# Performance work log

Hardware: AMD Instinct MI355X
Metric: run time of the kernel (lower is better)

Reference implementation:

```python
import jax, jax.numpy as jnp
import numpy as np

NX, NY, NZ = 432, 496, 1
VX, VY, VZ = 0.16, 0.16, 4.0
XOFF = VX / 2 + 0.0
YOFF = VY / 2 + (-39.68)
ZOFF = VZ / 2 + (-3.0)
GRID = NZ * NX * NY
P, NPT, B = 100000, 32, 8
EPS = 1e-3


def setup_inputs() -> dict:
    key = jax.random.key(0)
    k1, k2, k3, k4 = jax.random.split(key, 4)
    voxels = jax.random.normal(k1, (P, NPT, 4), dtype=jnp.float32)
    num_points = jax.random.randint(k2, (P,), 1, NPT + 1, dtype=jnp.int32)
    b = jax.random.randint(k3, (P,), 0, B, dtype=jnp.int32)
    # unique BEV cells (17 coprime with GRID, P < GRID) -> deterministic scatter
    cell = (jnp.arange(P, dtype=jnp.int32) * 17) % GRID
    y = cell // NX
    x = cell % NX
    coords = jnp.stack([b, jnp.zeros_like(b), y, x], axis=1)  # [P,4] (b,z,y,x)
    W = jax.random.normal(k4, (64, 10), dtype=jnp.float32) * 0.1
    gamma = jnp.ones((64,), dtype=jnp.float32)
    beta = jnp.zeros((64,), dtype=jnp.float32)
    return {"voxels": voxels, "num_points": num_points, "coords": coords,
            "W": W, "gamma": gamma, "beta": beta}


def reference(voxels, num_points, coords, W, gamma, beta):
    cf = coords.astype(voxels.dtype)
    npf = num_points.astype(voxels.dtype)
    # cluster feature: offset from pillar mean
    points_mean = voxels[:, :, :3].sum(axis=1, keepdims=True) / npf[:, None, None]
    f_cluster = voxels[:, :, :3] - points_mean
    # center feature: offset from voxel center
    cx = cf[:, 3, None] * VX + XOFF
    cy = cf[:, 2, None] * VY + YOFF
    cz = cf[:, 1, None] * VZ + ZOFF
    f_center = jnp.stack([voxels[:, :, 0] - cx,
                          voxels[:, :, 1] - cy,
                          voxels[:, :, 2] - cz], axis=-1)
    feat = jnp.concatenate([voxels, f_cluster, f_center], axis=-1)  # [P,N,10]
    mask = (jnp.arange(NPT, dtype=jnp.int32)[None, :] < num_points[:, None])
    feat = feat * mask.astype(feat.dtype)[:, :, None]
    # linear(10->64, no bias) + BatchNorm1d (batch stats, biased var) + relu
    x = jnp.einsum('pnf,cf->pnc', feat, W)  # [P,N,64]
    mean = x.mean(axis=(0, 1))
    var = ((x - mean) ** 2).mean(axis=(0, 1))
    x = (x - mean) * jax.lax.rsqrt(var + EPS) * gamma + beta
    x = jax.nn.relu(x)
    pillars = x.max(axis=1)  # [P,64]
    idx = coords[:, 1] + coords[:, 2] * NX + coords[:, 3]
    bev = jnp.zeros((B, GRID, 64), dtype=pillars.dtype)
    bev = bev.at[coords[:, 0], idx].set(pillars)
    bev = jnp.transpose(bev, (0, 2, 1))  # [B,64,GRID]
    return bev.reshape(B, 64 * NZ, NY, NX)
```

## Files before the change

kernel.cpp:

```cpp
#include <hip/hip_runtime.h>

typedef unsigned short u16;
typedef unsigned uint2n __attribute__((ext_vector_type(2)));
typedef float float4n __attribute__((ext_vector_type(4)));

#define NXg 432
#define NYg 496
#define GRIDg (NXg*NYg)
#define NPTg 32
#define Bg 8
#define CHg 64
#define NSLOT 32

__device__ __forceinline__ float bf2f(u16 u){
    union { unsigned int i; float f; } x; x.i = ((unsigned int)u) << 16; return x.f;
}
__device__ __forceinline__ u16 f2bf(float f){
    union { float f; unsigned int i; } x; x.f = f;
    unsigned int i = x.i + 0x7FFFu + ((x.i >> 16) & 1u);
    return (u16)(i >> 16);
}
__device__ __forceinline__ bool is_bf16(const void* gamma){
    return ((*(const unsigned*)gamma) & 0xFFFFu) != 0u;
}

__global__ __launch_bounds__(256) void pfe_init(int* __restrict__ map, float* __restrict__ chsum){
    int t = blockIdx.x*256 + threadIdx.x;
    ((int4*)map)[t] = make_int4(-1,-1,-1,-1);
    if (t < (NSLOT*128)/4) ((float4*)chsum)[t] = make_float4(0.f,0.f,0.f,0.f);
}

__global__ __launch_bounds__(256) void pfe_pillar(
    const void* __restrict__ vox, const int* __restrict__ nump,
    const int* __restrict__ coords, const void* __restrict__ Wv,
    const void* __restrict__ gv,
    void* __restrict__ pv, int* __restrict__ map, float* __restrict__ chsum,
    int P, int nwaves)
{
    const bool isbf = is_bf16(gv);
    int lane = threadIdx.x & 63;
    int wl   = __builtin_amdgcn_readfirstlane(threadIdx.x >> 6);
    int wid  = blockIdx.x*4 + wl;
    int n    = lane & 31;

    float w4,w5,w6,w7,w8,w9, wp0,wp1,wp2,wp3;
    bool gsel;
    {
        float w[10];
#pragma unroll
        for (int j=0;j<10;j++)
            w[j] = isbf ? bf2f(((const u16*)Wv)[lane*10 + j]) : ((const float*)Wv)[lane*10 + j];
        wp0 = w[0]+w[4]+w[7];
        wp1 = w[1]+w[5]+w[8];
        wp2 = w[2]+w[6]+w[9];
        wp3 = w[3];
        w4=w[4]; w5=w[5]; w6=w[6]; w7=w[7]; w8=w[8]; w9=w[9];
        float g = isbf ? bf2f(((const u16*)gv)[lane]) : ((const float*)gv)[lane];
        gsel = (g >= 0.f);
    }

    float sx = 0.f, sx2 = 0.f;

    for (int p = wid; p < P; p += nwaves) {
        int np = nump[p];
        int4 cc = *(const int4*)(coords + 4*p);

        float4 pt;
        if (isbf){
            ushort4 raw = *(const ushort4*)((const u16*)vox + ((size_t)p*NPTg + n)*4);
            pt = make_float4(bf2f(raw.x), bf2f(raw.y), bf2f(raw.z), bf2f(raw.w));
        } else {
            pt = *(const float4*)((const float*)vox + ((size_t)p*NPTg + n)*4);
        }
        float s0 = pt.x, s1 = pt.y, s2 = pt.z;
#pragma unroll
        for (int m = 1; m < 32; m <<= 1){
            s0 += __shfl_xor(s0, m, 64);
            s1 += __shfl_xor(s1, m, 64);
            s2 += __shfl_xor(s2, m, 64);
        }
        float inv = 1.0f / (float)np;
        float m0 = s0*inv, m1 = s1*inv, m2 = s2*inv;
        float ccx = (float)cc.w * 0.16f + 0.08f;
        float ccy = (float)cc.z * 0.16f + (0.08f - 39.68f);
        float ccz = (float)cc.y * 4.0f  + (2.0f - 3.0f);
        float d = -(m0*w4 + m1*w5 + m2*w6 + ccx*w7 + ccy*w8 + ccz*w9);

        float qmx = -3e38f, qmn = 3e38f, sq = 0.f, sq2 = 0.f;
#define PROC(ax,ay,az,aw) { \
        float q = fmaf((ax), wp0, fmaf((ay), wp1, fmaf((az), wp2, (aw)*wp3))); \
        qmx = fmaxf(qmx, q); qmn = fminf(qmn, q); \
        sq += q; sq2 = fmaf(q, q, sq2); }
        if (isbf){
            const ushort4* rg = (const ushort4*)vox + (size_t)p*NPTg;
            int k = 0;
            for (; k + 4 <= np; k += 4){
                ushort4 r0 = rg[k+0], r1 = rg[k+1], r2 = rg[k+2], r3 = rg[k+3];
                PROC(bf2f(r0.x), bf2f(r0.y), bf2f(r0.z), bf2f(r0.w));
                PROC(bf2f(r1.x), bf2f(r1.y), bf2f(r1.z), bf2f(r1.w));
                PROC(bf2f(r2.x), bf2f(r2.y), bf2f(r2.z), bf2f(r2.w));
                PROC(bf2f(r3.x), bf2f(r3.y), bf2f(r3.z), bf2f(r3.w));
            }
            for (; k < np; k++){
                ushort4 r = rg[k];
                PROC(bf2f(r.x), bf2f(r.y), bf2f(r.z), bf2f(r.w));
            }
        } else {
            const float4* rg = (const float4*)vox + (size_t)p*NPTg;
            int k = 0;
            for (; k + 4 <= np; k += 4){
                float4 a0 = rg[k+0], a1 = rg[k+1], a2 = rg[k+2], a3 = rg[k+3];
                PROC(a0.x,a0.y,a0.z,a0.w);
                PROC(a1.x,a1.y,a1.z,a1.w);
                PROC(a2.x,a2.y,a2.z,a2.w);
                PROC(a3.x,a3.y,a3.z,a3.w);
            }
            for (; k < np; k++){
                float4 a = rg[k];
                PROC(a.x,a.y,a.z,a.w);
            }
        }
#undef PROC

        float npf = (float)np;
        sx  += sq + npf*d;
        sx2 += sq2 + d*(2.f*sq + npf*d);

        float fmx = qmx + d, fmn = qmn + d;
        if (np < NPTg){ fmx = fmaxf(fmx, 0.f); fmn = fminf(fmn, 0.f); }
        float sel = gsel ? fmx : fmn;
        if (isbf) ((u16*)pv)[(size_t)p*CHg + lane] = f2bf(sel);
        else      ((float*)pv)[(size_t)p*CHg + lane] = sel;
        if (lane == 0) map[cc.x*GRIDg + cc.z*NXg + cc.w] = p;
    }

    float* slot = chsum + (blockIdx.x & (NSLOT-1))*128;
    atomicAdd(slot + lane, sx);
    atomicAdd(slot + 64 + lane, sx2);
}

__global__ __launch_bounds__(64) void pfe_stats(
    const float* __restrict__ chsum,
    const void* __restrict__ gv, const void* __restrict__ bv,
    float* __restrict__ sb, int P)
{
    const bool isbf = is_bf16(gv);
    int t = threadIdx.x;
    float S = 0.f, S2 = 0.f;
    for (int sl = 0; sl < NSLOT; sl++){
        S  += chsum[sl*128 + t];
        S2 += chsum[sl*128 + 64 + t];
    }
    float cnt = (float)P * (float)NPTg;
    float mean = S / cnt;
    float var  = S2 / cnt - mean*mean;
    float g  = isbf ? bf2f(((const u16*)gv)[t]) : ((const float*)gv)[t];
    float be = isbf ? bf2f(((const u16*)bv)[t]) : ((const float*)bv)[t];
    float sc = g * rsqrtf(var + 1e-3f);
    sb[t] = sc; sb[64 + t] = be - mean*sc;
}

__global__ __launch_bounds__(192) void pfe_gather(
    const int* __restrict__ map, const void* __restrict__ pv,
    const float* __restrict__ sb, const void* __restrict__ gv,
    void* __restrict__ out)
{
    const bool isbf = is_bf16(gv);
    int b  = blockIdx.z;
    int c0 = blockIdx.y * 32;
    int px = blockIdx.x*768 + threadIdx.x*4;
    int4 m4 = *(const int4*)(map + (size_t)b*GRIDg + px);
    bool v0 = m4.x >= 0, v1 = m4.y >= 0, v2 = m4.z >= 0, v3 = m4.w >= 0;
    int p0 = v0 ? m4.x : 0;
    int p1 = v1 ? m4.y : 0;
    int p2 = v2 ? m4.z : 0;
    int p3 = v3 ? m4.w : 0;

    if (isbf){
        const u16* pvh = (const u16*)pv;
        const uint4* r0 = (const uint4*)(pvh + (size_t)p0*CHg + c0);
        const uint4* r1 = (const uint4*)(pvh + (size_t)p1*CHg + c0);
        const uint4* r2 = (const uint4*)(pvh + (size_t)p2*CHg + c0);
        const uint4* r3 = (const uint4*)(pvh + (size_t)p3*CHg + c0);
        uint4 A0=r0[0], A1=r0[1], A2=r0[2], A3=r0[3];
        uint4 B0=r1[0], B1=r1[1], B2=r1[2], B3=r1[3];
        uint4 C0=r2[0], C1=r2[1], C2=r2[2], C3=r2[3];
        uint4 D0=r3[0], D1=r3[1], D2=r3[2], D3=r3[3];
        u16* ob = (u16*)out + ((size_t)(b*CHg + c0))*GRIDg + px;
#define GETB(Q0,Q1,Q2,Q3, COMP, CREL) { \
        unsigned w0=Q0.COMP, w1=Q1.COMP, w2=Q2.COMP, w3=Q3.COMP; \
        float sce = sb[c0+(CREL)],   bie = sb[64+c0+(CREL)]; \
        float sco = sb[c0+(CREL)+1], bio = sb[64+c0+(CREL)+1]; \
        float e0 = v0 ? fmaxf(fmaf(sce, bf2f((u16)(w0 & 0xFFFFu)), bie), 0.f) : 0.f; \
        float e1 = v1 ? fmaxf(fmaf(sce, bf2f((u16)(w1 & 0xFFFFu)), bie), 0.f) : 0.f; \
        float e2 = v2 ? fmaxf(fmaf(sce, bf2f((u16)(w2 & 0xFFFFu)), bie), 0.f) : 0.f; \
        float e3 = v3 ? fmaxf(fmaf(sce, bf2f((u16)(w3 & 0xFFFFu)), bie), 0.f) : 0.f; \
        float o0 = v0 ? fmaxf(fmaf(sco, bf2f((u16)(w0 >> 16)), bio), 0.f) : 0.f; \
        float o1 = v1 ? fmaxf(fmaf(sco, bf2f((u16)(w1 >> 16)), bio), 0.f) : 0.f; \
        float o2 = v2 ? fmaxf(fmaf(sco, bf2f((u16)(w2 >> 16)), bio), 0.f) : 0.f; \
        float o3 = v3 ? fmaxf(fmaf(sco, bf2f((u16)(w3 >> 16)), bio), 0.f) : 0.f; \
        uint2n pe, po; \
        pe.x = (unsigned)f2bf(e0) | ((unsigned)f2bf(e1) << 16); \
        pe.y = (unsigned)f2bf(e2) | ((unsigned)f2bf(e3) << 16); \
        po.x = (unsigned)f2bf(o0) | ((unsigned)f2bf(o1) << 16); \
        po.y = (unsigned)f2bf(o2) | ((unsigned)f2bf(o3) << 16); \
        __builtin_nontemporal_store(pe, (uint2n*)(ob + (size_t)(CREL)*GRIDg)); \
        __builtin_nontemporal_store(po, (uint2n*)(ob + (size_t)((CREL)+1)*GRIDg)); }
        GETB(A0,B0,C0,D0, x, 0)  GETB(A0,B0,C0,D0, y, 2)  GETB(A0,B0,C0,D0, z, 4)  GETB(A0,B0,C0,D0, w, 6)
        GETB(A1,B1,C1,D1, x, 8)  GETB(A1,B1,C1,D1, y, 10) GETB(A1,B1,C1,D1, z, 12) GETB(A1,B1,C1,D1, w, 14)
        GETB(A2,B2,C2,D2, x, 16) GETB(A2,B2,C2,D2, y, 18) GETB(A2,B2,C2,D2, z, 20) GETB(A2,B2,C2,D2, w, 22)
        GETB(A3,B3,C3,D3, x, 24) GETB(A3,B3,C3,D3, y, 26) GETB(A3,B3,C3,D3, z, 28) GETB(A3,B3,C3,D3, w, 30)
#undef GETB
    } else {
        const float* pvf = (const float*)pv;
        const float4* r0 = (const float4*)(pvf + (size_t)p0*CHg + c0);
        const float4* r1 = (const float4*)(pvf + (size_t)p1*CHg + c0);
        const float4* r2 = (const float4*)(pvf + (size_t)p2*CHg + c0);
        const float4* r3 = (const float4*)(pvf + (size_t)p3*CHg + c0);
        float* obf = (float*)out + ((size_t)(b*CHg + c0))*GRIDg + px;
#define LANEF(aq,bq,cq,dq, L, CREL) { \
        float sc = sb[c0+(CREL)], bi = sb[64+c0+(CREL)]; \
        float4n o; \
        o.x = v0 ? fmaxf(fmaf(sc, aq.L, bi), 0.f) : 0.f; \
        o.y = v1 ? fmaxf(fmaf(sc, bq.L, bi), 0.f) : 0.f; \
        o.z = v2 ? fmaxf(fmaf(sc, cq.L, bi), 0.f) : 0.f; \
        o.w = v3 ? fmaxf(fmaf(sc, dq.L, bi), 0.f) : 0.f; \
        __builtin_nontemporal_store(o, (float4n*)(obf + (size_t)(CREL)*GRIDg)); }
#define GETJ(J) { \
        float4 aq = r0[J], bq = r1[J], cq = r2[J], dq = r3[J]; \
        LANEF(aq,bq,cq,dq, x, 4*(J)+0) \
        LANEF(aq,bq,cq,dq, y, 4*(J)+1) \
        LANEF(aq,bq,cq,dq, z, 4*(J)+2) \
        LANEF(aq,bq,cq,dq, w, 4*(J)+3) }
        GETJ(0) GETJ(1) GETJ(2) GETJ(3) GETJ(4) GETJ(5) GETJ(6) GETJ(7)
#undef GETJ
#undef LANEF
    }
}

extern "C" void kernel_launch(void* const* d_in, const int* in_sizes, int n_in,
                              void* d_out, int out_size, void* d_ws, size_t ws_size,
                              hipStream_t stream)
{
    const void* vox   = d_in[0];
    const int* nump   = (const int*)d_in[1];
    const int* coords = (const int*)d_in[2];
    const void* Wv    = d_in[3];
    const void* gv    = d_in[4];
    const void* bv    = d_in[5];
    int P = in_sizes[1];

    float* chsum = (float*)d_ws;
    float* sb    = (float*)((char*)d_ws + 16384);
    void*  pv    = (void*)((char*)d_ws + 32768);
    int*   map   = (int*)((char*)pv + (size_t)P*CHg*4);

    int initThreads = (Bg*GRIDg)/4;
    pfe_init<<<initThreads/256, 256, 0, stream>>>(map, chsum);

    int blocks1 = 4096;
    pfe_pillar<<<blocks1, 256, 0, stream>>>(vox, nump, coords, Wv, gv, pv, map, chsum, P, blocks1*4);

    pfe_stats<<<1, 64, 0, stream>>>(chsum, gv, bv, sb, P);

    dim3 g3(GRIDg/768, 2, Bg);
    pfe_gather<<<g3, 192, 0, stream>>>(map, pv, sb, gv, d_out);
    pfe_gather<<<g3, 192, 0, stream>>>(map, pv, sb, gv, d_out);
}
```

Before: 595.8 us.

## Fuse BN stats into pillar kernel, drop duplicate gather, split max accumulators

Folds the batch-norm statistics reduction into the pillar kernel using a last-block-done atomic counter, which removes the separate single-block stats launch. Drops the second, redundant launch of the gather kernel, so the large BEV output is written once instead of twice. In the inner loop the per-channel weights are pre-multiplied by the sign of gamma, so only a running max is tracked instead of both max and min. The per-pillar accumulation is also split into two independent accumulator chains to expose more instruction-level parallelism. The last-block pattern adds a threadfence and an atomic per block, and relies on correct memory ordering for the chsum reads.

```diff
diff --git a/kernel.cpp b/kernel.cpp
--- a/kernel.cpp
+++ b/kernel.cpp
@@ -24,17 +24,20 @@
     return ((*(const unsigned*)gamma) & 0xFFFFu) != 0u;
 }
 
-__global__ __launch_bounds__(256) void pfe_init(int* __restrict__ map, float* __restrict__ chsum){
+__global__ __launch_bounds__(256) void pfe_init(int* __restrict__ map, float* __restrict__ chsum,
+                                                int* __restrict__ done){
     int t = blockIdx.x*256 + threadIdx.x;
     ((int4*)map)[t] = make_int4(-1,-1,-1,-1);
     if (t < (NSLOT*128)/4) ((float4*)chsum)[t] = make_float4(0.f,0.f,0.f,0.f);
+    if (t == 0) *done = 0;
 }
 
 __global__ __launch_bounds__(256) void pfe_pillar(
     const void* __restrict__ vox, const int* __restrict__ nump,
     const int* __restrict__ coords, const void* __restrict__ Wv,
-    const void* __restrict__ gv,
+    const void* __restrict__ gv, const void* __restrict__ bv,
     void* __restrict__ pv, int* __restrict__ map, float* __restrict__ chsum,
+    float* __restrict__ sb, int* __restrict__ done,
     int P, int nwaves)
 {
     const bool isbf = is_bf16(gv);
@@ -43,20 +46,22 @@
     int wid  = blockIdx.x*4 + wl;
     int n    = lane & 31;
 
-    float w4,w5,w6,w7,w8,w9, wp0,wp1,wp2,wp3;
-    bool gsel;
+    float w4,w5,w6,w7,w8,w9, vn0,vn1,vn2,vn3;
+    bool gsel; float sgn;
     {
         float w[10];
 #pragma unroll
         for (int j=0;j<10;j++)
             w[j] = isbf ? bf2f(((const u16*)Wv)[lane*10 + j]) : ((const float*)Wv)[lane*10 + j];
-        wp0 = w[0]+w[4]+w[7];
-        wp1 = w[1]+w[5]+w[8];
-        wp2 = w[2]+w[6]+w[9];
-        wp3 = w[3];
+        float wp0 = w[0]+w[4]+w[7];
+        float wp1 = w[1]+w[5]+w[8];
+        float wp2 = w[2]+w[6]+w[9];
+        float wp3 = w[3];
         w4=w[4]; w5=w[5]; w6=w[6]; w7=w[7]; w8=w[8]; w9=w[9];
         float g = isbf ? bf2f(((const u16*)gv)[lane]) : ((const float*)gv)[lane];
         gsel = (g >= 0.f);
+        sgn  = gsel ? 1.f : -1.f;
+        vn0 = wp0*sgn; vn1 = wp1*sgn; vn2 = wp2*sgn; vn3 = wp3*sgn;
     }
 
     float sx = 0.f, sx2 = 0.f;
@@ -86,78 +91,90 @@
         float ccz = (float)cc.y * 4.0f  + (2.0f - 3.0f);
         float d = -(m0*w4 + m1*w5 + m2*w6 + ccx*w7 + ccy*w8 + ccz*w9);
 
-        float qmx = -3e38f, qmn = 3e38f, sq = 0.f, sq2 = 0.f;
-#define PROC(ax,ay,az,aw) { \
-        float q = fmaf((ax), wp0, fmaf((ay), wp1, fmaf((az), wp2, (aw)*wp3))); \
-        qmx = fmaxf(qmx, q); qmn = fminf(qmn, q); \
-        sq += q; sq2 = fmaf(q, q, sq2); }
+        float qmA = -3e38f, qmB = -3e38f, sqA = 0.f, sqB = 0.f, s2A = 0.f, s2B = 0.f;
+#define PROCA(ax,ay,az,aw) { \
+        float q = fmaf((ax), vn0, fmaf((ay), vn1, fmaf((az), vn2, (aw)*vn3))); \
+        qmA = fmaxf(qmA, q); sqA += q; s2A = fmaf(q, q, s2A); }
+#define PROCB(ax,ay,az,aw) { \
+        float q = fmaf((ax), vn0, fmaf((ay), vn1, fmaf((az), vn2, (aw)*vn3))); \
+        qmB = fmaxf(qmB, q); sqB += q; s2B = fmaf(q, q, s2B); }
         if (isbf){
             const ushort4* rg = (const ushort4*)vox + (size_t)p*NPTg;
             int k = 0;
             for (; k + 4 <= np; k += 4){
                 ushort4 r0 = rg[k+0], r1 = rg[k+1], r2 = rg[k+2], r3 = rg[k+3];
-                PROC(bf2f(r0.x), bf2f(r0.y), bf2f(r0.z), bf2f(r0.w));
-                PROC(bf2f(r1.x), bf2f(r1.y), bf2f(r1.z), bf2f(r1.w));
-                PROC(bf2f(r2.x), bf2f(r2.y), bf2f(r2.z), bf2f(r2.w));
-                PROC(bf2f(r3.x), bf2f(r3.y), bf2f(r3.z), bf2f(r3.w));
+                PROCA(bf2f(r0.x), bf2f(r0.y), bf2f(r0.z), bf2f(r0.w));
+                PROCB(bf2f(r1.x), bf2f(r1.y), bf2f(r1.z), bf2f(r1.w));
+                PROCA(bf2f(r2.x), bf2f(r2.y), bf2f(r2.z), bf2f(r2.w));
+                PROCB(bf2f(r3.x), bf2f(r3.y), bf2f(r3.z), bf2f(r3.w));
             }
             for (; k < np; k++){
                 ushort4 r = rg[k];
-                PROC(bf2f(r.x), bf2f(r.y), bf2f(r.z), bf2f(r.w));
+                PROCA(bf2f(r.x), bf2f(r.y), bf2f(r.z), bf2f(r.w));
             }
         } else {
             const float4* rg = (const float4*)vox + (size_t)p*NPTg;
             int k = 0;
             for (; k + 4 <= np; k += 4){
                 float4 a0 = rg[k+0], a1 = rg[k+1], a2 = rg[k+2], a3 = rg[k+3];
-                PROC(a0.x,a0.y,a0.z,a0.w);
-                PROC(a1.x,a1.y,a1.z,a1.w);
-                PROC(a2.x,a2.y,a2.z,a2.w);
-                PROC(a3.x,a3.y,a3.z,a3.w);
+                PROCA(a0.x,a0.y,a0.z,a0.w);
+                PROCB(a1.x,a1.y,a1.z,a1.w);
+                PROCA(a2.x,a2.y,a2.z,a2.w);
+                PROCB(a3.x,a3.y,a3.z,a3.w);
             }
             for (; k < np; k++){
                 float4 a = rg[k];
-                PROC(a.x,a.y,a.z,a.w);
-            }
-        }
-#undef PROC
+                PROCA(a.x,a.y,a.z,a.w);
+            }
+        }
+#undef PROCA
+#undef PROCB
+        float qmx = fmaxf(qmA, qmB);
+        float sqp = sqA + sqB;
+        float sq2 = s2A + s2B;
+        float sq  = gsel ? sqp : -sqp;
 
         float npf = (float)np;
         sx  += sq + npf*d;
         sx2 += sq2 + d*(2.f*sq + npf*d);
 
-        float fmx = qmx + d, fmn = qmn + d;
-        if (np < NPTg){ fmx = fmaxf(fmx, 0.f); fmn = fminf(fmn, 0.f); }
-        float sel = gsel ? fmx : fmn;
-        if (isbf) ((u16*)pv)[(size_t)p*CHg + lane] = f2bf(sel);
-        else      ((float*)pv)[(size_t)p*CHg + lane] = sel;
+        float ext = gsel ? qmx : -qmx;
+        float f = ext + d;
+        if (np < NPTg) f = gsel ? fmaxf(f, 0.f) : fminf(f, 0.f);
+        if (isbf) ((u16*)pv)[(size_t)p*CHg + lane] = f2bf(f);
+        else      ((float*)pv)[(size_t)p*CHg + lane] = f;
         if (lane == 0) map[cc.x*GRIDg + cc.z*NXg + cc.w] = p;
     }
 
     float* slot = chsum + (blockIdx.x & (NSLOT-1))*128;
     atomicAdd(slot + lane, sx);
     atomicAdd(slot + 64 + lane, sx2);
-}
-
-__global__ __launch_bounds__(64) void pfe_stats(
-    const float* __restrict__ chsum,
-    const void* __restrict__ gv, const void* __restrict__ bv,
-    float* __restrict__ sb, int P)
-{
-    const bool isbf = is_bf16(gv);
-    int t = threadIdx.x;
-    float S = 0.f, S2 = 0.f;
-    for (int sl = 0; sl < NSLOT; sl++){
-        S  += chsum[sl*128 + t];
-        S2 += chsum[sl*128 + 64 + t];
-    }
-    float cnt = (float)P * (float)NPTg;
-    float mean = S / cnt;
-    float var  = S2 / cnt - mean*mean;
-    float g  = isbf ? bf2f(((const u16*)gv)[t]) : ((const float*)gv)[t];
-    float be = isbf ? bf2f(((const u16*)bv)[t]) : ((const float*)bv)[t];
-    float sc = g * rsqrtf(var + 1e-3f);
-    sb[t] = sc; sb[64 + t] = be - mean*sc;
+
+    __shared__ int isLast;
+    __threadfence();
+    if (threadIdx.x == 0){
+        int c = atomicAdd(done, 1);
+        isLast = (c == (int)gridDim.x - 1);
+    }
+    __syncthreads();
+    if (isLast){
+        __threadfence();
+        int t = threadIdx.x;
+        if (t < 64){
+            float S = 0.f, S2 = 0.f;
+            for (int sl = 0; sl < NSLOT; sl++){
+                S  += chsum[sl*128 + t];
+                S2 += chsum[sl*128 + 64 + t];
+            }
+            float cnt = (float)P * (float)NPTg;
+            float mean = S / cnt;
+            float var  = S2 / cnt - mean*mean;
+            float g  = isbf ? bf2f(((const u16*)gv)[t]) : ((const float*)gv)[t];
+            float be = isbf ? bf2f(((const u16*)bv)[t]) : ((const float*)bv)[t];
+            float sc = g * rsqrtf(var + 1e-3f);
+            sb[t] = sc; sb[64 + t] = be - mean*sc;
+        }
+    }
 }
 
 __global__ __launch_bounds__(192) void pfe_gather(
@@ -252,18 +269,17 @@
 
     float* chsum = (float*)d_ws;
     float* sb    = (float*)((char*)d_ws + 16384);
+    int*   done  = (int*)((char*)d_ws + 16384 + 512);
     void*  pv    = (void*)((char*)d_ws + 32768);
     int*   map   = (int*)((char*)pv + (size_t)P*CHg*4);
 
     int initThreads = (Bg*GRIDg)/4;
-    pfe_init<<<initThreads/256, 256, 0, stream>>>(map, chsum);
+    pfe_init<<<initThreads/256, 256, 0, stream>>>(map, chsum, done);
 
     int blocks1 = 4096;
-    pfe_pillar<<<blocks1, 256, 0, stream>>>(vox, nump, coords, Wv, gv, pv, map, chsum, P, blocks1*4);
-
-    pfe_stats<<<1, 64, 0, stream>>>(chsum, gv, bv, sb, P);
+    pfe_pillar<<<blocks1, 256, 0, stream>>>(vox, nump, coords, Wv, gv, bv,
+                                            pv, map, chsum, sb, done, P, blocks1*4);
 
     dim3 g3(GRIDg/768, 2, Bg);
     pfe_gather<<<g3, 192, 0, stream>>>(map, pv, sb, gv, d_out);
-    pfe_gather<<<g3, 192, 0, stream>>>(map, pv, sb, gv, d_out);
-}
+}
```

Result: slower. 947.5 us (+59.0%).
